# Performance work log

Hardware: AMD Instinct MI355X
Metric: run time of the kernel (lower is better)

Reference implementation:

```python
import jax, jax.numpy as jnp
import numpy as np
import math

D_MODEL = 256
D_STATE = 16
D_CONV = 4
EXPAND = 2
N_HEADS = 4
D_INNER = EXPAND * D_MODEL          # 512
DT_RANK = (D_MODEL + 15) // 16      # 16
B_SZ, SEQ = 4, 2048


def setup_inputs() -> dict:
    key = jax.random.key(0)
    ks = jax.random.split(key, 12)
    rn = lambda i, shp, sc=0.02: jax.random.normal(ks[i], shp, dtype=jnp.float32) * sc
    x = jax.random.normal(ks[0], (B_SZ, SEQ, D_MODEL), dtype=jnp.float32)
    return dict(
        x=x,
        ln_g=jnp.ones((D_MODEL,), jnp.float32),
        ln_b=jnp.zeros((D_MODEL,), jnp.float32),
        W_in=rn(1, (D_MODEL, 2 * D_INNER)),
        conv_w=rn(2, (D_INNER, D_CONV), 0.1),
        conv_b=jnp.zeros((D_INNER,), jnp.float32),
        W_xproj=rn(3, (D_INNER, DT_RANK + 2 * D_STATE)),
        W_dt=rn(4, (DT_RANK, D_INNER), 0.1),
        b_dt=jnp.full((D_INNER,), -4.6, jnp.float32),  # softplus ~ 0.01 init
        A_log=jnp.log(jnp.tile(jnp.arange(1, D_STATE + 1, dtype=jnp.float32), (D_INNER, 1))),
        Dp=jnp.ones((D_INNER,), jnp.float32),
        W_out_m=rn(5, (D_INNER, D_MODEL)),
        W_qkv=rn(6, (D_MODEL, 3 * D_MODEL)),
        b_qkv=jnp.zeros((3 * D_MODEL,), jnp.float32),
        W_o=rn(7, (D_MODEL, D_MODEL)),
        b_o=jnp.zeros((D_MODEL,), jnp.float32),
        W_gate=rn(8, (2 * D_MODEL, D_MODEL)),
        b_gate=jnp.zeros((D_MODEL,), jnp.float32),
    )


def _sssd_forward(x, ln_g, ln_b, W_in, conv_w, conv_b, W_xproj, W_dt, b_dt,
                  A_log, Dp, W_out_m, W_qkv, b_qkv, W_o, b_o, W_gate, b_gate):
    B, L, D = x.shape
    # LayerNorm
    mu = x.mean(-1, keepdims=True)
    var = x.var(-1, keepdims=True)
    xn = (x - mu) * jax.lax.rsqrt(var + 1e-5) * ln_g + ln_b

    # ---- Mamba branch ----
    xz = xn @ W_in                      # (B,L,2*D_INNER)
    xm, z = jnp.split(xz, 2, axis=-1)
    # causal depthwise conv1d (kernel D_CONV)
    xp = jnp.pad(xm, ((0, 0), (D_CONV - 1, 0), (0, 0)))
    xc = conv_b + sum(xp[:, k:k + L, :] * conv_w[:, k] for k in range(D_CONV))
    xc = jax.nn.silu(xc)
    dbl = xc @ W_xproj                  # (B,L,DT_RANK+2*D_STATE)
    dt_in = dbl[..., :DT_RANK]
    Bm = dbl[..., DT_RANK:DT_RANK + D_STATE]
    Cm = dbl[..., DT_RANK + D_STATE:]
    dt = jax.nn.softplus(dt_in @ W_dt + b_dt)   # (B,L,D_INNER)
    A = -jnp.exp(A_log)                 # (D_INNER, D_STATE)

    def step(h, inp):
        x_t, dt_t, B_t, C_t = inp       # (B,Din),(B,Din),(B,N),(B,N)
        dA = jnp.exp(dt_t[..., None] * A)               # (B,Din,N)
        h = dA * h + (dt_t * x_t)[..., None] * B_t[:, None, :]
        y = jnp.einsum('bdn,bn->bd', h, C_t)
        return h, y

    h0 = jnp.zeros((B, D_INNER, D_STATE), x.dtype)
    xs = (jnp.swapaxes(xc, 0, 1), jnp.swapaxes(dt, 0, 1),
          jnp.swapaxes(Bm, 0, 1), jnp.swapaxes(Cm, 0, 1))
    _, ys = jax.lax.scan(step, h0, xs)
    y = jnp.swapaxes(ys, 0, 1) + xc * Dp
    y = y * jax.nn.silu(z)
    ssm_out = y @ W_out_m               # (B,L,D)

    # ---- MHSA branch (eval: no dropout) ----
    hd = D // N_HEADS
    qkv = xn @ W_qkv + b_qkv
    q, k, v = jnp.split(qkv, 3, axis=-1)
    sh = lambda t: t.reshape(B, L, N_HEADS, hd).transpose(0, 2, 1, 3)
    q, k, v = sh(q), sh(k), sh(v)
    scores = jnp.einsum('bhqd,bhkd->bhqk', q, k) * (1.0 / math.sqrt(hd))
    attn = jax.nn.softmax(scores, axis=-1)
    o = jnp.einsum('bhqk,bhkd->bhqd', attn, v).transpose(0, 2, 1, 3).reshape(B, L, D)
    attn_out = o @ W_o + b_o

    # ---- sigmoid gate fusion ----
    gate = jax.nn.sigmoid(jnp.concatenate([ssm_out, attn_out], axis=-1) @ W_gate + b_gate)
    fused = gate * ssm_out + (1.0 - gate) * attn_out
    return x + fused


def reference(x, ln_g, ln_b, W_in, conv_w, conv_b, W_xproj, W_dt, b_dt,
              A_log, Dp, W_out_m, W_qkv, b_qkv, W_o, b_o, W_gate, b_gate):
    return _sssd_forward(x, ln_g, ln_b, W_in, conv_w, conv_b, W_xproj, W_dt, b_dt,
                         A_log, Dp, W_out_m, W_qkv, b_qkv, W_o, b_o, W_gate, b_gate)
```

## Files before the change

### kernel.cpp

```cpp
#include <hip/hip_runtime.h>
#include <math.h>

#define B_SZ 4
#define SEQ 2048
#define DM 256
#define DI 512
#define DS 16
#define DTR 16
#define NH 4
#define HD 64
#define T_TOK (B_SZ*SEQ)
#define NCH 64
#define CL (SEQ/NCH)
#define QSCALE 0.18033688f

typedef short bf16x8 __attribute__((ext_vector_type(8)));
typedef float f32x4  __attribute__((ext_vector_type(4)));
typedef float f32x16 __attribute__((ext_vector_type(16)));
typedef unsigned short u16;

__device__ __forceinline__ float sigmoidf_(float x){ return 1.f/(1.f+__expf(-x)); }
__device__ __forceinline__ u16 f2bf(float x){
  unsigned int u = __float_as_uint(x);
  u += 0x7fffu + ((u>>16)&1u);
  return (u16)(u>>16);
}
__device__ __forceinline__ float bf2f(u16 u){ return __uint_as_float(((unsigned)u)<<16); }
__device__ __forceinline__ unsigned cvt_pk_bf16(float lo, float hi){
  unsigned r;
  asm("v_cvt_pk_bf16_f32 %0, %1, %2" : "=v"(r) : "v"(lo), "v"(hi));
  return r;
}
__device__ __forceinline__ void permswap(unsigned &a, unsigned &b){
  asm volatile("v_permlane32_swap_b32 %0, %1" : "+v"(a), "+v"(b));
}
__device__ __forceinline__ float xor32f(float v){
  unsigned a = __float_as_uint(v), b = a;
  permswap(a, b);
  return __uint_as_float(a);
}

struct TcvtArgs {
  const float* src[6];
  u16* dst[6];
  int K[6];
  int Nvalid[6];
  int Npad[6];
};
__global__ __launch_bounds__(256) void tcvt_all(TcvtArgs a) {
  int wi = blockIdx.z;
  int K = a.K[wi], Nv = a.Nvalid[wi], Np = a.Npad[wi];
  int k0 = blockIdx.x*64, n0 = blockIdx.y*64;
  if (k0 >= K || n0 >= Np) return;
  __shared__ u16 tile[64][65];
  const float* src = a.src[wi];
  u16* dst = a.dst[wi];
  int tn = threadIdx.x & 63, tq = threadIdx.x >> 6;
#pragma unroll
  for (int j=0;j<16;++j){
    int kk = j*4 + tq;
    int n = n0 + tn;
    tile[tn][kk] = (n < Nv) ? f2bf(src[(size_t)(k0+kk)*Nv + n]) : (u16)0;
  }
  __syncthreads();
#pragma unroll
  for (int j=0;j<16;++j){
    int nn = j*4 + tq;
    dst[(size_t)(n0+nn)*K + k0 + tn] = tile[nn][tn];
  }
}

__global__ __launch_bounds__(256) void ln_kernel(const float* __restrict__ x,
    const float* __restrict__ g, const float* __restrict__ b,
    u16* __restrict__ xn_bf) {
  int wid = threadIdx.x >> 6;
  int lane = threadIdx.x & 63;
  int token = blockIdx.x*4 + wid;
  const float* xr = x + (size_t)token*DM;
  float4 v = *(const float4*)&xr[lane*4];
  float s  = v.x+v.y+v.z+v.w;
  float ss = v.x*v.x+v.y*v.y+v.z*v.z+v.w*v.w;
  for (int m=1;m<64;m<<=1){ s += __shfl_xor(s,m); ss += __shfl_xor(ss,m); }
  float mu  = s * (1.f/DM);
  float var = ss*(1.f/DM) - mu*mu;
  float rs  = rsqrtf(var + 1e-5f);
  float4 gv = *(const float4*)&g[lane*4];
  float4 bv = *(const float4*)&b[lane*4];
  uint2 o;
  o.x = cvt_pk_bf16((v.x-mu)*rs*gv.x + bv.x, (v.y-mu)*rs*gv.y + bv.y);
  o.y = cvt_pk_bf16((v.z-mu)*rs*gv.z + bv.z, (v.w-mu)*rs*gv.w + bv.w);
  *(uint2*)&xn_bf[(size_t)token*DM + lane*4] = o;
}

template<int ACT>
__global__ __launch_bounds__(256) void gemm_mfma(const u16* __restrict__ A,
    const u16* __restrict__ Wt, const float* __restrict__ bias,
    float* __restrict__ C, u16* __restrict__ Cbf, int K, int ldc, int nvalid,
    int qcols, float qscale, const float* __restrict__ xres,
    const float* __restrict__ cat2, u16* __restrict__ vTout,
    u16* __restrict__ qkvout) {
  __shared__ u16 lds[12288];
  int tid = threadIdx.x;
  int m0 = blockIdx.y*128, n0 = blockIdx.x*64;
  int w = tid>>6, l = tid&63, lq = l&15, lg = l>>4;
  int wm = w>>1, wn = w&1;
  f32x4 acc[4][2] = {};
  for (int k0 = 0; k0 < K; k0 += 64) {
#pragma unroll
    for (int i=0;i<4;++i){
      int gid = i*256 + tid;
      int row = gid>>3, g = gid&7;
      *(bf16x8*)&lds[row*64 + ((g ^ (row&7))*8)] =
          *(const bf16x8*)&A[(size_t)(m0+row)*K + k0 + g*8];
    }
#pragma unroll
    for (int i=0;i<2;++i){
      int gid = i*256 + tid;
      int row = gid>>3, g = gid&7;
      *(bf16x8*)&lds[8192 + row*64 + ((g ^ (row&7))*8)] =
          *(const bf16x8*)&Wt[(size_t)(n0+row)*K + k0 + g*8];
    }
    __syncthreads();
#pragma unroll
    for (int ks=0;ks<2;++ks){
      bf16x8 af[4], bfv[2];
#pragma unroll
      for (int mi=0;mi<4;++mi){
        int row = wm*64 + mi*16 + lq;
        af[mi] = *(bf16x8*)&lds[row*64 + (((ks*4+lg) ^ (row&7))*8)];
      }
#pragma unroll
      for (int nj=0;nj<2;++nj){
        int row = wn*32 + nj*16 + lq;
        bfv[nj] = *(bf16x8*)&lds[8192 + row*64 + (((ks*4+lg) ^ (row&7))*8)];
      }
#pragma unroll
      for (int mi=0;mi<4;++mi)
#pragma unroll
        for (int nj=0;nj<2;++nj)
          acc[mi][nj] = __builtin_amdgcn_mfma_f32_16x16x32_bf16(af[mi], bfv[nj], acc[mi][nj], 0,0,0);
    }
    __syncthreads();
  }
#pragma unroll
  for (int mi=0;mi<4;++mi){
#pragma unroll
    for (int nj=0;nj<2;++nj){
#pragma unroll
      for (int r=0;r<4;++r){
        int row = m0 + wm*64 + mi*16 + lg*4 + r;
        int col = n0 + wn*32 + nj*16 + lq;
        if (col < nvalid) {
          float v = acc[mi][nj][r];
          if (ACT!=5 && bias) v += bias[col];
          if (col < qcols) v *= qscale;
          if (ACT==2) {
            float g = sigmoidf_(v);
            float sv = cat2[(size_t)row*512 + col];
            float av = cat2[(size_t)row*512 + 256 + col];
            C[(size_t)row*256 + col] = xres[(size_t)row*256 + col] + g*sv + (1.f-g)*av;
          } else if (ACT==5) {
            if (col < 1024) {
              Cbf[(size_t)row*1024 + col] = f2bf(v);
            } else {
              int c2 = col - 1024;
              v += bias[c2];
              if (c2 < 256) v *= qscale;
              qkvout[(size_t)row*768 + c2] = f2bf(v);
              if (c2 >= 512) {
                int bb = row>>11, ll = row&2047;
                int hh = (c2-512)>>6, dd = (c2-512)&63;
                vTout[(((size_t)(bb*4+hh))*64 + dd)*SEQ + ll] = f2bf(v);
              }
            }
          } else {
            if (ACT==1) v = sigmoidf_(v);
            if (C)   C[(size_t)row*ldc + col] = v;
            if (Cbf) Cbf[(size_t)row*ldc + col] = f2bf(v);
          }
        }
      }
    }
  }
}

__global__ __launch_bounds__(256) void conv_kernel(const u16* __restrict__ xzb,
    const float* __restrict__ cw, const float* __restrict__ cb,
    u16* __restrict__ xc_bf) {
  int idx = blockIdx.x*256 + threadIdx.x;
  int d2 = (idx & 255)*2;
  int t = idx >> 8;
  int l = t & (SEQ-1);
  float acc0 = cb[d2], acc1 = cb[d2+1];
  float4 wA = *(const float4*)&cw[d2*4];
  float4 wB = *(const float4*)&cw[d2*4+4];
  const u16* base = xzb + (size_t)t*1024 + d2;
  ushort2 v;
  if (l>=3){ v = *(const ushort2*)&base[-3*1024]; acc0 += bf2f(v.x)*wA.x; acc1 += bf2f(v.y)*wB.x; }
  if (l>=2){ v = *(const ushort2*)&base[-2*1024]; acc0 += bf2f(v.x)*wA.y; acc1 += bf2f(v.y)*wB.y; }
  if (l>=1){ v = *(const ushort2*)&base[-1*1024]; acc0 += bf2f(v.x)*wA.z; acc1 += bf2f(v.y)*wB.z; }
  v = *(const ushort2*)&base[0];
  acc0 += bf2f(v.x)*wA.w; acc1 += bf2f(v.y)*wB.w;
  float r0 = acc0 * sigmoidf_(acc0);
  float r1 = acc1 * sigmoidf_(acc1);
  *(unsigned*)&xc_bf[(size_t)t*DI + d2] = cvt_pk_bf16(r0, r1);
}

__global__ __launch_bounds__(256) void dt_kernel(const float* __restrict__ dbl,
    const float* __restrict__ Wdt, const float* __restrict__ bdt,
    u16* __restrict__ dt) {
  __shared__ float sdbl[4][16];
  int wid = threadIdx.x>>6, lane = threadIdx.x&63;
  int token = blockIdx.x*4 + wid;
  if (lane < 16) sdbl[wid][lane] = dbl[(size_t)token*48 + lane];
  __syncthreads();
  float din[16];
#pragma unroll
  for (int k=0;k<16;++k) din[k] = sdbl[wid][k];
#pragma unroll
  for (int r=0;r<8;++r){
    int d = lane + r*64;
    float acc = bdt[d];
#pragma unroll
    for (int k=0;k<16;++k) acc += din[k]*Wdt[k*DI+d];
    float sp = (acc > 20.f) ? acc : log1pf(__expf(acc));
    dt[(size_t)token*DI+d] = f2bf(sp);
  }
}

__global__ __launch_bounds__(512) void scan_p1(const u16* __restrict__ xc_bf,
    const u16* __restrict__ dt, const float* __restrict__ dbl,
    const float* __restrict__ A_log, u16* __restrict__ Pws, u16* __restrict__ Hws) {
  __shared__ float sB[CL][16];
  int d = threadIdx.x;
  int bc = blockIdx.x;
  int b = bc >> 6, c = bc & 63;
  {
    int t = threadIdx.x >> 4, n = threadIdx.x & 15;
    sB[t][n] = dbl[((size_t)b*SEQ + c*CL + t)*48 + DTR + n];
  }
  __syncthreads();
  float An[16];
#pragma unroll
  for (int i=0;i<4;++i){
    float4 a = *(const float4*)&A_log[d*16 + i*4];
    An[i*4+0] = -__expf(a.x); An[i*4+1] = -__expf(a.y);
    An[i*4+2] = -__expf(a.z); An[i*4+3] = -__expf(a.w);
  }
  float h[16] = {};
  float P[16];
#pragma unroll
  for (int n=0;n<16;++n) P[n] = 1.f;
  size_t tok = (size_t)b*SEQ + c*CL;
  for (int t=0;t<CL;++t,++tok){
    float dtv = bf2f(dt[tok*DI+d]);
    float xcv = bf2f(xc_bf[tok*DI+d]);
    float u = dtv*xcv;
    float4 B0 = *(float4*)&sB[t][0];
    float4 B1 = *(float4*)&sB[t][4];
    float4 B2 = *(float4*)&sB[t][8];
    float4 B3 = *(float4*)&sB[t][12];
    float Bv[16] = {B0.x,B0.y,B0.z,B0.w,B1.x,B1.y,B1.z,B1.w,
                    B2.x,B2.y,B2.z,B2.w,B3.x,B3.y,B3.z,B3.w};
#pragma unroll
    for (int n=0;n<16;++n){
      float e = __expf(dtv*An[n]);
      P[n] *= e;
      h[n] = e*h[n] + u*Bv[n];
    }
  }
  size_t base = (((size_t)b*NCH + c)*DI + d)*16;
#pragma unroll
  for (int i=0;i<8;++i){
    *(unsigned*)&Pws[base + i*2] = cvt_pk_bf16(P[i*2], P[i*2+1]);
    *(unsigned*)&Hws[base + i*2] = cvt_pk_bf16(h[i*2], h[i*2+1]);
  }
}

__global__ __launch_bounds__(256) void scan_combine(const u16* __restrict__ Pws,
    const u16* __restrict__ Hws, u16* __restrict__ H0ws) {
  int gid = blockIdx.x*256 + threadIdx.x;
  int b  = gid >> 13;
  int dn = gid & 8191;
  float h0 = 0.f;
#pragma unroll 4
  for (int c=0;c<NCH;++c){
    size_t idx = ((size_t)(b*NCH+c)<<13) + dn;
    H0ws[idx] = f2bf(h0);
    h0 = bf2f(Pws[idx])*h0 + bf2f(Hws[idx]);
  }
}

__global__ __launch_bounds__(512) void scan_p2(const u16* __restrict__ xc_bf,
    const u16* __restrict__ dt, const float* __restrict__ dbl,
    const float* __restrict__ A_log, const float* __restrict__ Dp,
    const u16* __restrict__ xzb, const u16* __restrict__ H0ws,
    u16* __restrict__ ygate_bf) {
  __shared__ float sBC[CL][32];
  int d = threadIdx.x;
  int bc = blockIdx.x;
  int b = bc >> 6, c = bc & 63;
#pragma unroll
  for (int i=0;i<2;++i){
    int idx = i*512 + threadIdx.x;
    int t = idx >> 5, q = idx & 31;
    sBC[t][q] = dbl[((size_t)b*SEQ + c*CL + t)*48 + DTR + q];
  }
  __syncthreads();
  float An[16];
#pragma unroll
  for (int i=0;i<4;++i){
    float4 a = *(const float4*)&A_log[d*16 + i*4];
    An[i*4+0] = -__expf(a.x); An[i*4+1] = -__expf(a.y);
    An[i*4+2] = -__expf(a.z); An[i*4+3] = -__expf(a.w);
  }
  float Dd = Dp[d];
  float h[16];
  size_t base = (((size_t)b*NCH + c)*DI + d)*16;
  {
    bf16x8 h8a = *(const bf16x8*)&H0ws[base];
    bf16x8 h8b = *(const bf16x8*)&H0ws[base+8];
#pragma unroll
    for (int n=0;n<8;++n){ h[n] = bf2f((u16)h8a[n]); h[8+n] = bf2f((u16)h8b[n]); }
  }
  size_t tok = (size_t)b*SEQ + c*CL;
  for (int t=0;t<CL;++t,++tok){
    float dtv = bf2f(dt[tok*DI+d]);
    float xcv = bf2f(xc_bf[tok*DI+d]);
    float zv  = bf2f(xzb[tok*1024 + DI + d]);
    float u = dtv*xcv;
    float4 B0 = *(float4*)&sBC[t][0];
    float4 B1 = *(float4*)&sBC[t][4];
    float4 B2 = *(float4*)&sBC[t][8];
    float4 B3 = *(float4*)&sBC[t][12];
    float4 C0 = *(float4*)&sBC[t][16];
    float4 C1 = *(float4*)&sBC[t][20];
    float4 C2 = *(float4*)&sBC[t][24];
    float4 C3 = *(float4*)&sBC[t][28];
    float Bv[16] = {B0.x,B0.y,B0.z,B0.w,B1.x,B1.y,B1.z,B1.w,
                    B2.x,B2.y,B2.z,B2.w,B3.x,B3.y,B3.z,B3.w};
    float Cv[16] = {C0.x,C0.y,C0.z,C0.w,C1.x,C1.y,C1.z,C1.w,
                    C2.x,C2.y,C2.z,C2.w,C3.x,C3.y,C3.z,C3.w};
    float y = 0.f;
#pragma unroll
    for (int n=0;n<16;++n){
      float e = __expf(dtv*An[n]);
      h[n] = e*h[n] + u*Bv[n];
      y += h[n]*Cv[n];
    }
    y += xcv*Dd;
    ygate_bf[tok*DI + d] = f2bf(y * (zv*sigmoidf_(zv)));
  }
}

__global__ __launch_bounds__(256) void attn_mfma_kernel(const u16* __restrict__ qkvb,
    const u16* __restrict__ vT,
    u16* __restrict__ Opart, float* __restrict__ ml) {
  __shared__ u16 lds[8192];
  int H = blockIdx.x + 8*blockIdx.y + 128*(int)blockIdx.z;
  int cx = H & 7, kk = H >> 3;
  int xq = kk & 7;
  int G  = cx*8 + (kk >> 3);
  int bh = G & 15, s = G >> 4;
  int b = bh>>2, h = bh&3;
  int tid = threadIdx.x;
  int w = tid>>6, l = tid&63;
  int lo32 = l & 31;
  int hi = l >> 5;
  size_t bbase = (size_t)b*SEQ;
  size_t vbase = (size_t)bh*HD*SEQ;
  int q_base = xq*256 + w*64;

  bf16x8 qf[2][4];
#pragma unroll
  for (int qg=0; qg<2; ++qg)
#pragma unroll
    for (int dsl=0; dsl<4; ++dsl)
      qf[qg][dsl] = *(const bf16x8*)&qkvb[(bbase + q_base + qg*32 + lo32)*768 + h*HD + dsl*16 + hi*8];

  float m_[2] = {-1e30f,-1e30f}, l_[2] = {0.f,0.f};
  f32x16 oacc[2][2] = {};

  int srow = tid>>3, sg = tid&7;
  int kt0 = s*8;
  bf16x8 kreg[2], vreg[2];

#define LOADT(kt) { \
  kreg[0] = *(const bf16x8*)&qkvb[(bbase + (size_t)(kt)*64 + srow)*768 + 256 + h*HD + sg*8]; \
  kreg[1] = *(const bf16x8*)&qkvb[(bbase + (size_t)(kt)*64 + srow + 32)*768 + 256 + h*HD + sg*8]; \
  vreg[0] = *(const bf16x8*)&vT[vbase + (size_t)srow*SEQ + (kt)*64 + sg*8]; \
  vreg[1] = *(const bf16x8*)&vT[vbase + (size_t)(srow+32)*SEQ + (kt)*64 + sg*8]; }
#define STORET() { \
  *(bf16x8*)&lds[srow*64 + ((sg ^ (srow&7))*8)] = kreg[0]; \
  *(bf16x8*)&lds[(srow+32)*64 + ((sg ^ ((srow+32)&7))*8)] = kreg[1]; \
  *(bf16x8*)&lds[4096 + srow*64 + ((sg ^ (srow&7))*8)] = vreg[0]; \
  *(bf16x8*)&lds[4096 + (srow+32)*64 + ((sg ^ ((srow+32)&7))*8)] = vreg[1]; }
#define EXCH(X, Y, s_own, s_oth) { \
  unsigned xa = (X), yb = (Y); \
  permswap(xa, yb); \
  s_own = (l < 32) ? (X) : xa; \
  s_oth = (l < 32) ? yb : (Y); }

  LOADT(kt0);
  for (int it=0; it<8; ++it){
    __syncthreads();
    STORET();
    __syncthreads();
    if (it < 7) LOADT(kt0+it+1);

#pragma unroll
    for (int t32=0; t32<2; ++t32){
      int krow = t32*32 + lo32;
      bf16x8 kf[4];
#pragma unroll
      for (int dsl=0; dsl<4; ++dsl)
        kf[dsl] = *(bf16x8*)&lds[krow*64 + (((dsl*2 + hi) ^ (krow&7))*8)];

      bf16x8 pf[2][2];
#pragma unroll
      for (int qg=0; qg<2; ++qg){
        f32x16 sacc = {0,0,0,0,0,0,0,0,0,0,0,0,0,0,0,0};
#pragma unroll
        for (int dsl=0; dsl<4; ++dsl)
          sacc = __builtin_amdgcn_mfma_f32_32x32x16_bf16(kf[dsl], qf[qg][dsl], sacc, 0,0,0);

        float tm = sacc[0];
#pragma unroll
        for (int r=1;r<16;++r) tm = fmaxf(tm, sacc[r]);
        tm = fmaxf(tm, xor32f(tm));
        if (__any(tm - m_[qg] > 8.f)) {
          float mn = fmaxf(m_[qg], tm);
          float sc = exp2f(m_[qg] - mn);
          m_[qg] = mn;
          l_[qg] *= sc;
#pragma unroll
          for (int r=0;r<16;++r){ oacc[qg][0][r] *= sc; oacc[qg][1][r] *= sc; }
        }
        float p[16];
        float ps = 0.f;
#pragma unroll
        for (int r=0;r<16;++r){ p[r] = exp2f(sacc[r] - m_[qg]); ps += p[r]; }
        ps += xor32f(ps);
        l_[qg] += ps;

        unsigned A0 = cvt_pk_bf16(p[0],p[1]),  A1 = cvt_pk_bf16(p[2],p[3]);
        unsigned B0 = cvt_pk_bf16(p[4],p[5]),  B1 = cvt_pk_bf16(p[6],p[7]);
        unsigned C0 = cvt_pk_bf16(p[8],p[9]),  C1 = cvt_pk_bf16(p[10],p[11]);
        unsigned D0 = cvt_pk_bf16(p[12],p[13]),D1 = cvt_pk_bf16(p[14],p[15]);
        unsigned s0,s1,s2,s3,s4,s5,s6,s7;
        EXCH(A0,B0,s0,s2); EXCH(A1,B1,s1,s3);
        EXCH(C0,D0,s4,s6); EXCH(C1,D1,s5,s7);
        ((unsigned*)&pf[qg][0])[0]=s0; ((unsigned*)&pf[qg][0])[1]=s1;
        ((unsigned*)&pf[qg][0])[2]=s2; ((unsigned*)&pf[qg][0])[3]=s3;
        ((unsigned*)&pf[qg][1])[0]=s4; ((unsigned*)&pf[qg][1])[1]=s5;
        ((unsigned*)&pf[qg][1])[2]=s6; ((unsigned*)&pf[qg][1])[3]=s7;
      }

#pragma unroll
      for (int dtile=0; dtile<2; ++dtile){
        int vrow = dtile*32 + lo32;
        bf16x8 vf0 = *(bf16x8*)&lds[4096 + vrow*64 + (((t32*4 + 0 + hi) ^ (vrow&7))*8)];
        bf16x8 vf1 = *(bf16x8*)&lds[4096 + vrow*64 + (((t32*4 + 2 + hi) ^ (vrow&7))*8)];
        oacc[0][dtile] = __builtin_amdgcn_mfma_f32_32x32x16_bf16(vf0, pf[0][0], oacc[0][dtile], 0,0,0);
        oacc[0][dtile] = __builtin_amdgcn_mfma_f32_32x32x16_bf16(vf1, pf[0][1], oacc[0][dtile], 0,0,0);
        oacc[1][dtile] = __builtin_amdgcn_mfma_f32_32x32x16_bf16(vf0, pf[1][0], oacc[1][dtile], 0,0,0);
        oacc[1][dtile] = __builtin_amdgcn_mfma_f32_32x32x16_bf16(vf1, pf[1][1], oacc[1][dtile], 0,0,0);
      }
    }
  }
#undef LOADT
#undef STORET
#undef EXCH

  int sidx = bh*4 + s;
#pragma unroll
  for (int qg=0; qg<2; ++qg){
    size_t rb = ((size_t)sidx*SEQ + q_base + qg*32 + lo32)*64;
#pragma unroll
    for (int dtile=0; dtile<2; ++dtile){
#pragma unroll
      for (int rg=0; rg<4; ++rg){
        uint2 pk;
        pk.x = cvt_pk_bf16(oacc[qg][dtile][rg*4+0], oacc[qg][dtile][rg*4+1]);
        pk.y = cvt_pk_bf16(oacc[qg][dtile][rg*4+2], oacc[qg][dtile][rg*4+3]);
        *(uint2*)&Opart[rb + dtile*32 + rg*8 + 4*hi] = pk;
      }
    }
    if (l < 32){
      ml[((size_t)sidx*SEQ + q_base + qg*32 + lo32)*2    ] = m_[qg];
      ml[((size_t)sidx*SEQ + q_base + qg*32 + lo32)*2 + 1] = l_[qg];
    }
  }
}

__global__ __launch_bounds__(256) void attn_merge_kernel(const u16* __restrict__ Opart,
    const float* __restrict__ ml, u16* __restrict__ attn_bf) {
  int w = threadIdx.x>>6, lane = threadIdx.x&63;
  int R = blockIdx.x*4 + w;
  int bh = R>>11, q = R&2047;
  float m[4], lv[4];
#pragma unroll
  for (int s=0;s<4;++s){
    m[s]  = ml[((size_t)(bh*4+s)*SEQ + q)*2];
    lv[s] = ml[((size_t)(bh*4+s)*SEQ + q)*2 + 1];
  }
  float ms = fmaxf(fmaxf(m[0],m[1]),fmaxf(m[2],m[3]));
  float o = 0.f, lsum = 0.f;
#pragma unroll
  for (int s=0;s<4;++s){
    float wsc = exp2f(m[s]-ms);
    lsum += wsc*lv[s];
    o += wsc*bf2f(Opart[((size_t)(bh*4+s)*SEQ + q)*64 + lane]);
  }
  size_t token = (size_t)(bh>>2)*SEQ + q;
  attn_bf[token*DM + (bh&3)*HD + lane] = f2bf(o/lsum);
}

extern "C" void kernel_launch(void* const* d_in, const int* in_sizes, int n_in,
                              void* d_out, int out_size, void* d_ws, size_t ws_size,
                              hipStream_t stream) {
  const float* x      = (const float*)d_in[0];
  const float* ln_g   = (const float*)d_in[1];
  const float* ln_b   = (const float*)d_in[2];
  const float* W_in   = (const float*)d_in[3];
  const float* conv_w = (const float*)d_in[4];
  const float* conv_b = (const float*)d_in[5];
  const float* W_xproj= (const float*)d_in[6];
  const float* W_dt   = (const float*)d_in[7];
  const float* b_dt   = (const float*)d_in[8];
  const float* A_log  = (const float*)d_in[9];
  const float* Dp     = (const float*)d_in[10];
  const float* W_out_m= (const float*)d_in[11];
  const float* W_qkv  = (const float*)d_in[12];
  const float* b_qkv  = (const float*)d_in[13];
  const float* W_o    = (const float*)d_in[14];
  const float* b_o    = (const float*)d_in[15];
  const float* W_gate = (const float*)d_in[16];
  const float* b_gate = (const float*)d_in[17];
  float* out = (float*)d_out;

  float* ws = (float*)d_ws;
  u16*   xn_bf   = (u16*)(ws);
  u16*   xzb     = (u16*)(ws + 1048576);
  u16*   qkv_bf  = (u16*)(ws + 9437184);
  u16*   xc_bf   = (u16*)(ws + 12582912);
  float* dblb    = ws + 16777216;
  u16*   dtb     = (u16*)(ws + 17170432);
  u16*   ygate_bf= (u16*)(ws + 21364736);
  u16*   attn_bf = (u16*)(ws + 23461888);
  float* catb    = ws + 24510464;
  u16*   catb_bf = (u16*)(ws + 28704768);
  float* gateb   = ws + 30801920;
  u16*   Wt_all  = (u16*)(ws + 32899072);
  u16*   Opart = (u16*)(ws + 1048576);
  float* mlb   = (float*)xn_bf;
  u16*   vTb   = (u16*)gateb;
  u16*   Pws   = (u16*)catb;
  u16*   Hws   = (u16*)(catb + 1048576);
  u16*   H0ws  = (u16*)(catb + 2097152);

  u16* Wt_in   = Wt_all;
  u16* Wt_qkv  = Wt_all + 262144;
  u16* Wt_out  = Wt_all + 458752;
  u16* Wt_o    = Wt_all + 589824;
  u16* Wt_gate = Wt_all + 655360;
  u16* Wt_xp   = Wt_all + 786432;

  TcvtArgs ta;
  ta.src[0]=W_in;    ta.dst[0]=Wt_in;   ta.K[0]=256; ta.Nvalid[0]=1024; ta.Npad[0]=1024;
  ta.src[1]=W_qkv;   ta.dst[1]=Wt_qkv;  ta.K[1]=256; ta.Nvalid[1]=768;  ta.Npad[1]=768;
  ta.src[2]=W_out_m; ta.dst[2]=Wt_out;  ta.K[2]=512; ta.Nvalid[2]=256;  ta.Npad[2]=256;
  ta.src[3]=W_o;     ta.dst[3]=Wt_o;    ta.K[3]=256; ta.Nvalid[3]=256;  ta.Npad[3]=256;
  ta.src[4]=W_gate;  ta.dst[4]=Wt_gate; ta.K[4]=512; ta.Nvalid[4]=256;  ta.Npad[4]=256;
  ta.src[5]=W_xproj; ta.dst[5]=Wt_xp;   ta.K[5]=512; ta.Nvalid[5]=48;   ta.Npad[5]=64;
  tcvt_all<<<dim3(8,16,6), 256, 0, stream>>>(ta);

  ln_kernel<<<T_TOK/4, 256, 0, stream>>>(x, ln_g, ln_b, xn_bf);
  gemm_mfma<5><<<dim3(28,64), 256, 0, stream>>>(xn_bf, Wt_in, b_qkv, nullptr, xzb, 256, 0, 1792, 0, QSCALE, nullptr, nullptr, vTb, qkv_bf);
  conv_kernel<<<T_TOK, 256, 0, stream>>>(xzb, conv_w, conv_b, xc_bf);
  gemm_mfma<0><<<dim3(1,64), 256, 0, stream>>>(xc_bf, Wt_xp, nullptr, dblb, nullptr, 512, 48, 48, 0, 1.f, nullptr, nullptr, nullptr, nullptr);
  dt_kernel<<<T_TOK/4, 256, 0, stream>>>(dblb, W_dt, b_dt, dtb);
  scan_p1<<<B_SZ*NCH, 512, 0, stream>>>(xc_bf, dtb, dblb, A_log, Pws, Hws);
  scan_combine<<<128, 256, 0, stream>>>(Pws, Hws, H0ws);
  scan_p2<<<B_SZ*NCH, 512, 0, stream>>>(xc_bf, dtb, dblb, A_log, Dp, xzb, H0ws, ygate_bf);
  attn_mfma_kernel<<<dim3(8, 16, 4), 256, 0, stream>>>(qkv_bf, vTb, Opart, mlb);
  attn_merge_kernel<<<8192, 256, 0, stream>>>(Opart, mlb, attn_bf);
  gemm_mfma<0><<<dim3(4,64), 256, 0, stream>>>(ygate_bf, Wt_out, nullptr, catb, catb_bf, 512, 512, 256, 0, 1.f, nullptr, nullptr, nullptr, nullptr);
  gemm_mfma<0><<<dim3(4,64), 256, 0, stream>>>(attn_bf, Wt_o, b_o, catb+256, catb_bf+256, 256, 512, 256, 0, 1.f, nullptr, nullptr, nullptr, nullptr);
  gemm_mfma<2><<<dim3(4,64), 256, 0, stream>>>(catb_bf, Wt_gate, b_gate, out, nullptr, 512, 256, 256, 0, 1.f, x, catb, nullptr, nullptr);
}
```

Before: 243.0 us.

## Double attention key splits and merge the two output-projection GEMMs into one launch

Attention is now split over 8 key chunks instead of 4, each covering 4 key tiles. That doubles the block count to fill more CUs, and the merge kernel is generalised to combine NSP partials. The SSM out-projection and attention o-projection GEMMs now run in a single launch: a new ACT=6 mode picks operands by block column half and writes both halves of the concat buffer. The cost is twice the partial-output traffic in the merge step. It also relies on the workspace for Opart and ml being large enough for 8 splits.

New measurement: 239.0 us. About the same (-1.6%).

```diff
diff --git a/kernel.cpp b/kernel.cpp
--- a/kernel.cpp
+++ b/kernel.cpp
@@ -12,6 +12,7 @@
 #define T_TOK (B_SZ*SEQ)
 #define NCH 64
 #define CL (SEQ/NCH)
+#define NSP 8
 #define QSCALE 0.18033688f
 
 typedef short bf16x8 __attribute__((ext_vector_type(8)));
@@ -98,27 +99,37 @@
     float* __restrict__ C, u16* __restrict__ Cbf, int K, int ldc, int nvalid,
     int qcols, float qscale, const float* __restrict__ xres,
     const float* __restrict__ cat2, u16* __restrict__ vTout,
-    u16* __restrict__ qkvout) {
+    u16* __restrict__ qkvout,
+    const u16* __restrict__ A2, const u16* __restrict__ Wt2, int K2,
+    const float* __restrict__ bias2) {
   __shared__ u16 lds[12288];
   int tid = threadIdx.x;
-  int m0 = blockIdx.y*128, n0 = blockIdx.x*64;
+  int m0 = blockIdx.y*128;
+  int n0 = blockIdx.x*64;
+  const u16* Ap = A; const u16* Wp = Wt; int Kp = K; const float* bp = bias;
+  int halfsel = 0;
+  if (ACT==6){
+    halfsel = (blockIdx.x >= 4);
+    if (halfsel){ Ap = A2; Wp = Wt2; Kp = K2; bp = bias2; }
+    n0 = (blockIdx.x & 3)*64;
+  }
   int w = tid>>6, l = tid&63, lq = l&15, lg = l>>4;
   int wm = w>>1, wn = w&1;
   f32x4 acc[4][2] = {};
-  for (int k0 = 0; k0 < K; k0 += 64) {
+  for (int k0 = 0; k0 < Kp; k0 += 64) {
 #pragma unroll
     for (int i=0;i<4;++i){
       int gid = i*256 + tid;
       int row = gid>>3, g = gid&7;
       *(bf16x8*)&lds[row*64 + ((g ^ (row&7))*8)] =
-          *(const bf16x8*)&A[(size_t)(m0+row)*K + k0 + g*8];
+          *(const bf16x8*)&Ap[(size_t)(m0+row)*Kp + k0 + g*8];
     }
 #pragma unroll
     for (int i=0;i<2;++i){
       int gid = i*256 + tid;
       int row = gid>>3, g = gid&7;
       *(bf16x8*)&lds[8192 + row*64 + ((g ^ (row&7))*8)] =
-          *(const bf16x8*)&Wt[(size_t)(n0+row)*K + k0 + g*8];
+          *(const bf16x8*)&Wp[(size_t)(n0+row)*Kp + k0 + g*8];
     }
     __syncthreads();
 #pragma unroll
@@ -152,9 +163,10 @@
         int col = n0 + wn*32 + nj*16 + lq;
         if (col < nvalid) {
           float v = acc[mi][nj][r];
-          if (ACT!=5 && bias) v += bias[col];
+          if (ACT==0 && bias) v += bias[col];
           if (col < qcols) v *= qscale;
           if (ACT==2) {
+            if (bias) v += bias[col];
             float g = sigmoidf_(v);
             float sv = cat2[(size_t)row*512 + col];
             float av = cat2[(size_t)row*512 + 256 + col];
@@ -173,8 +185,11 @@
                 vTout[(((size_t)(bb*4+hh))*64 + dd)*SEQ + ll] = f2bf(v);
               }
             }
+          } else if (ACT==6) {
+            if (bp) v += bp[col];
+            C[(size_t)row*512 + halfsel*256 + col] = v;
+            Cbf[(size_t)row*512 + halfsel*256 + col] = f2bf(v);
           } else {
-            if (ACT==1) v = sigmoidf_(v);
             if (C)   C[(size_t)row*ldc + col] = v;
             if (Cbf) Cbf[(size_t)row*ldc + col] = f2bf(v);
           }
@@ -360,7 +375,7 @@
   int H = blockIdx.x + 8*blockIdx.y + 128*(int)blockIdx.z;
   int cx = H & 7, kk = H >> 3;
   int xq = kk & 7;
-  int G  = cx*8 + (kk >> 3);
+  int G  = cx*16 + (kk >> 3);
   int bh = G & 15, s = G >> 4;
   int b = bh>>2, h = bh&3;
   int tid = threadIdx.x;
@@ -382,7 +397,7 @@
   f32x16 oacc[2][2] = {};
 
   int srow = tid>>3, sg = tid&7;
-  int kt0 = s*8;
+  int kt0 = s*4;
   bf16x8 kreg[2], vreg[2];
 
 #define LOADT(kt) { \
@@ -402,11 +417,11 @@
   s_oth = (l < 32) ? yb : (Y); }
 
   LOADT(kt0);
-  for (int it=0; it<8; ++it){
+  for (int it=0; it<4; ++it){
     __syncthreads();
     STORET();
     __syncthreads();
-    if (it < 7) LOADT(kt0+it+1);
+    if (it < 3) LOADT(kt0+it+1);
 
 #pragma unroll
     for (int t32=0; t32<2; ++t32){
@@ -472,7 +487,7 @@
 #undef STORET
 #undef EXCH
 
-  int sidx = bh*4 + s;
+  int sidx = bh*NSP + s;
 #pragma unroll
   for (int qg=0; qg<2; ++qg){
     size_t rb = ((size_t)sidx*SEQ + q_base + qg*32 + lo32)*64;
@@ -498,19 +513,21 @@
   int w = threadIdx.x>>6, lane = threadIdx.x&63;
   int R = blockIdx.x*4 + w;
   int bh = R>>11, q = R&2047;
-  float m[4], lv[4];
-#pragma unroll
-  for (int s=0;s<4;++s){
-    m[s]  = ml[((size_t)(bh*4+s)*SEQ + q)*2];
-    lv[s] = ml[((size_t)(bh*4+s)*SEQ + q)*2 + 1];
-  }
-  float ms = fmaxf(fmaxf(m[0],m[1]),fmaxf(m[2],m[3]));
+  float m[NSP], lv[NSP];
+#pragma unroll
+  for (int s=0;s<NSP;++s){
+    m[s]  = ml[((size_t)(bh*NSP+s)*SEQ + q)*2];
+    lv[s] = ml[((size_t)(bh*NSP+s)*SEQ + q)*2 + 1];
+  }
+  float ms = m[0];
+#pragma unroll
+  for (int s=1;s<NSP;++s) ms = fmaxf(ms, m[s]);
   float o = 0.f, lsum = 0.f;
 #pragma unroll
-  for (int s=0;s<4;++s){
+  for (int s=0;s<NSP;++s){
     float wsc = exp2f(m[s]-ms);
     lsum += wsc*lv[s];
-    o += wsc*bf2f(Opart[((size_t)(bh*4+s)*SEQ + q)*64 + lane]);
+    o += wsc*bf2f(Opart[((size_t)(bh*NSP+s)*SEQ + q)*64 + lane]);
   }
   size_t token = (size_t)(bh>>2)*SEQ + q;
   attn_bf[token*DM + (bh&3)*HD + lane] = f2bf(o/lsum);
@@ -576,16 +593,15 @@
   tcvt_all<<<dim3(8,16,6), 256, 0, stream>>>(ta);
 
   ln_kernel<<<T_TOK/4, 256, 0, stream>>>(x, ln_g, ln_b, xn_bf);
-  gemm_mfma<5><<<dim3(28,64), 256, 0, stream>>>(xn_bf, Wt_in, b_qkv, nullptr, xzb, 256, 0, 1792, 0, QSCALE, nullptr, nullptr, vTb, qkv_bf);
+  gemm_mfma<5><<<dim3(28,64), 256, 0, stream>>>(xn_bf, Wt_in, b_qkv, nullptr, xzb, 256, 0, 1792, 0, QSCALE, nullptr, nullptr, vTb, qkv_bf, nullptr, nullptr, 0, nullptr);
   conv_kernel<<<T_TOK, 256, 0, stream>>>(xzb, conv_w, conv_b, xc_bf);
-  gemm_mfma<0><<<dim3(1,64), 256, 0, stream>>>(xc_bf, Wt_xp, nullptr, dblb, nullptr, 512, 48, 48, 0, 1.f, nullptr, nullptr, nullptr, nullptr);
+  gemm_mfma<0><<<dim3(1,64), 256, 0, stream>>>(xc_bf, Wt_xp, nullptr, dblb, nullptr, 512, 48, 48, 0, 1.f, nullptr, nullptr, nullptr, nullptr, nullptr, nullptr, 0, nullptr);
   dt_kernel<<<T_TOK/4, 256, 0, stream>>>(dblb, W_dt, b_dt, dtb);
   scan_p1<<<B_SZ*NCH, 512, 0, stream>>>(xc_bf, dtb, dblb, A_log, Pws, Hws);
   scan_combine<<<128, 256, 0, stream>>>(Pws, Hws, H0ws);
   scan_p2<<<B_SZ*NCH, 512, 0, stream>>>(xc_bf, dtb, dblb, A_log, Dp, xzb, H0ws, ygate_bf);
-  attn_mfma_kernel<<<dim3(8, 16, 4), 256, 0, stream>>>(qkv_bf, vTb, Opart, mlb);
+  attn_mfma_kernel<<<dim3(8, 16, 8), 256, 0, stream>>>(qkv_bf, vTb, Opart, mlb);
   attn_merge_kernel<<<8192, 256, 0, stream>>>(Opart, mlb, attn_bf);
-  gemm_mfma<0><<<dim3(4,64), 256, 0, stream>>>(ygate_bf, Wt_out, nullptr, catb, catb_bf, 512, 512, 256, 0, 1.f, nullptr, nullptr, nullptr, nullptr);
-  gemm_mfma<0><<<dim3(4,64), 256, 0, stream>>>(attn_bf, Wt_o, b_o, catb+256, catb_bf+256, 256, 512, 256, 0, 1.f, nullptr, nullptr, nullptr, nullptr);
-  gemm_mfma<2><<<dim3(4,64), 256, 0, stream>>>(catb_bf, Wt_gate, b_gate, out, nullptr, 512, 256, 256, 0, 1.f, x, catb, nullptr, nullptr);
-}
+  gemm_mfma<6><<<dim3(8,64), 256, 0, stream>>>(ygate_bf, Wt_out, nullptr, catb, catb_bf, 512, 512, 256, 0, 1.f, nullptr, nullptr, nullptr, nullptr, attn_bf, Wt_o, 256, b_o);
+  gemm_mfma<2><<<dim3(4,64), 256, 0, stream>>>(catb_bf, Wt_gate, b_gate, out, nullptr, 512, 256, 256, 0, 1.f, x, catb, nullptr, nullptr, nullptr, nullptr, 0, b_gate);
+}
```
